# Performance work log

Measured on AMD Instinct MI355X. Metric: run time of the kernel, lower is better.

## Reference

```python
import jax, jax.numpy as jnp
import numpy as np

N_NODES = 50000
N_EDGES = 800000
IN_SIZE = 1024
EMB = 500


def setup_inputs() -> dict:
    key = jax.random.key(0)
    ks = jax.random.split(key, 9)
    x = jax.random.uniform(ks[0], (N_NODES, IN_SIZE), dtype=jnp.float32)
    edge_index = jax.random.randint(ks[1], (2, N_EDGES), 0, N_NODES, dtype=jnp.int32)
    edge_weight = jax.random.uniform(ks[2], (N_EDGES,), dtype=jnp.float32)
    s = 0.05
    wenc = jax.random.normal(ks[3], (EMB, IN_SIZE), dtype=jnp.float32) * s
    benc = jax.random.normal(ks[4], (EMB,), dtype=jnp.float32) * s
    wdec = jax.random.normal(ks[5], (IN_SIZE, EMB), dtype=jnp.float32) * s
    bdec = jax.random.normal(ks[6], (IN_SIZE,), dtype=jnp.float32) * s
    conv_weight = jax.random.normal(ks[7], (EMB, EMB), dtype=jnp.float32) * 0.1
    # lin.weight initialized N(0,0.1) + identity, per reset_parameters
    lin_weight = jax.random.normal(ks[8], (EMB, EMB), dtype=jnp.float32) * 0.1 + jnp.eye(EMB, dtype=jnp.float32)
    return {"x": x, "edge_index": edge_index, "edge_weight": edge_weight,
            "wenc": wenc, "benc": benc, "wdec": wdec, "bdec": bdec,
            "conv_weight": conv_weight, "lin_weight": lin_weight}


def reference(x, edge_index, edge_weight, wenc, benc, wdec, bdec, conv_weight, lin_weight):
    # encoder: h = sigmoid(x @ wenc^T + benc)          [N, EMB]
    h = jax.nn.sigmoid(x @ wenc.T + benc)
    # GraphConv (old PyG): neighbor transform then scatter-add to destinations
    h2 = h @ conv_weight                                # [N, EMB]
    src, dst = edge_index[0], edge_index[1]
    msgs = h2[src] * edge_weight[:, None]               # [E, EMB] gather + weight
    agg = jax.ops.segment_sum(msgs, dst, num_segments=x.shape[0])
    hout = agg + h @ lin_weight.T                       # root term via nn.Linear
    # decoder
    p = hout @ wdec.T + bdec                            # [N, IN_SIZE]
    return p
```

## Files before the change

kernel.cpp:

```cpp
#include <hip/hip_runtime.h>
#include <hip/hip_bf16.h>

typedef unsigned int u32;
typedef short bf16x8 __attribute__((ext_vector_type(8)));
typedef float floatx4 __attribute__((ext_vector_type(4)));

#define NNODES 50000
#define NEDGES 800000
#define INSZ   1024
#define EMB    500
#define EMBP   512

__device__ __forceinline__ short f2bf(float f) {
    u32 u = __builtin_bit_cast(u32, f);
    u32 r = u + 0x7FFFu + ((u >> 16) & 1u);
    return (short)(r >> 16);
}
__device__ __forceinline__ float bf2f(short h) {
    u32 u = ((u32)(unsigned short)h) << 16;
    return __builtin_bit_cast(float, u);
}

#define GLDS16(gp, lp) __builtin_amdgcn_global_load_lds( \
    (const __attribute__((address_space(1))) u32*)(gp),  \
    (__attribute__((address_space(3))) u32*)(lp), 16, 0, 0)

__device__ __forceinline__ u32 xcd_swz(u32 orig, u32 q, u32 r) {
    u32 xcd = orig & 7u, seq = orig >> 3;
    u32 base = (xcd < r) ? xcd * (q + 1u) : r * (q + 1u) + (xcd - r) * q;
    return base + seq;
}

__global__ void pack_all(const float* __restrict__ wenc, const float* __restrict__ conv,
                         const float* __restrict__ lin,  const float* __restrict__ wdec,
                         short* __restrict__ wencP, short* __restrict__ Wmid,
                         short* __restrict__ wdecP) {
    int tid = blockIdx.x * 256 + threadIdx.x;
    {
        int m = tid >> 10, k = tid & 1023;
        wencP[tid] = (m < EMB) ? f2bf(wenc[m * INSZ + k]) : (short)0;
    }
    {
        int m = tid >> 10, k = tid & 1023;
        short v = 0;
        if (m < EMB) {
            if (k < EMBP) { if (k < EMB) v = f2bf(conv[k * EMB + m]); }
            else          { int kk = k - EMBP; if (kk < EMB) v = f2bf(lin[m * EMB + kk]); }
        }
        Wmid[tid] = v;
    }
    {
        int m = tid >> 9, k = tid & 511;
        wdecP[tid] = (k < EMB) ? f2bf(wdec[m * EMB + k]) : (short)0;
    }
}

__global__ __launch_bounds__(256)
void conv_x(const float* __restrict__ X, short* __restrict__ Xb) {
    size_t base = ((size_t)blockIdx.x * 256 + threadIdx.x) * 8;
    floatx4 f0 = *(const floatx4*)(X + base);
    floatx4 f1 = *(const floatx4*)(X + base + 4);
    bf16x8 p;
#pragma unroll
    for (int j = 0; j < 4; ++j) { p[j] = f2bf(f0[j]); p[4 + j] = f2bf(f1[j]); }
    *(bf16x8*)(Xb + base) = p;
}


__global__ __launch_bounds__(256)
void gemm_enc(const short* __restrict__ Xb, const short* __restrict__ Wp,
              const float* __restrict__ benc, short* __restrict__ H) {
    __shared__ short As[2][128 * 32];
    __shared__ short Bs[2][128 * 32];
    const int tid  = threadIdx.x;
    const int lane = tid & 63;
    const int wave = tid >> 6;
    const int wr   = (wave >> 1) * 64;
    const int wc   = (wave & 1) * 64;
    const u32 swz  = xcd_swz(blockIdx.y * 4 + blockIdx.x, 195, 4);
    const int rowBase = (int)(swz >> 2) * 128;
    const int colBase = (int)(swz & 3) * 128;

    floatx4 acc[4][4] = {};

    const int r0 = tid >> 2;
    const int c0 = (tid & 3) * 8;
    int ar0 = rowBase + r0;       if (ar0 >= NNODES) ar0 = NNODES - 1;
    int ar1 = rowBase + r0 + 64;  if (ar1 >= NNODES) ar1 = NNODES - 1;
    const short* aP0 = Xb + (size_t)ar0 * INSZ + c0;
    const short* aP1 = Xb + (size_t)ar1 * INSZ + c0;
    const short* bP0 = Wp + (size_t)(colBase + r0) * INSZ + c0;
    const short* bP1 = Wp + (size_t)(colBase + r0 + 64) * INSZ + c0;

    const int q8  = (lane >> 4) * 8;
    const int m16 = lane & 15;

#define STAGE_E(buf, k0)                                   \
    GLDS16(aP0 + (k0), &As[buf][tid * 8]);                 \
    GLDS16(aP1 + (k0), &As[buf][2048 + tid * 8]);          \
    GLDS16(bP0 + (k0), &Bs[buf][tid * 8]);                 \
    GLDS16(bP1 + (k0), &Bs[buf][2048 + tid * 8]);

    STAGE_E(0, 0);
    __syncthreads();
    int cur = 0;
    for (int t = 0; t < 32; ++t) {
        if (t + 1 < 32) { STAGE_E(cur ^ 1, (t + 1) * 32); }
        bf16x8 af[4], bfr[4];
#pragma unroll
        for (int i = 0; i < 4; ++i) {
            af[i]  = *(const bf16x8*)&As[cur][(wr + i * 16 + m16) * 32 + q8];
            bfr[i] = *(const bf16x8*)&Bs[cur][(wc + i * 16 + m16) * 32 + q8];
        }
#pragma unroll
        for (int i = 0; i < 4; ++i)
#pragma unroll
            for (int j = 0; j < 4; ++j)
                acc[i][j] = __builtin_amdgcn_mfma_f32_16x16x32_bf16(af[i], bfr[j], acc[i][j], 0, 0, 0);
        __syncthreads();
        cur ^= 1;
    }
#undef STAGE_E

    const int rq = (lane >> 4) * 4;
#pragma unroll
    for (int i = 0; i < 4; ++i)
#pragma unroll
        for (int j = 0; j < 4; ++j)
#pragma unroll
            for (int reg = 0; reg < 4; ++reg) {
                int row = rowBase + wr + i * 16 + rq + reg;
                int col = colBase + wc + j * 16 + m16;
                if (row < NNODES) {
                    float b = (col < EMB) ? benc[col] : 0.f;
                    float v = 1.f / (1.f + __expf(-(acc[i][j][reg] + b)));
                    H[(size_t)row * EMBP + col] = f2bf(v);
                }
            }
}

__global__ __launch_bounds__(256)
void gemm_mid(const short* __restrict__ AggB, const short* __restrict__ H,
              const short* __restrict__ Wm, short* __restrict__ Hout) {
    __shared__ short As[2][128 * 32];
    __shared__ short Bs[2][128 * 32];
    const int tid  = threadIdx.x;
    const int lane = tid & 63;
    const int wave = tid >> 6;
    const int wr   = (wave >> 1) * 64;
    const int wc   = (wave & 1) * 64;
    const u32 swz  = xcd_swz(blockIdx.y * 4 + blockIdx.x, 195, 4);
    const int rowBase = (int)(swz >> 2) * 128;
    const int colBase = (int)(swz & 3) * 128;

    floatx4 acc[4][4] = {};

    const int r0 = tid >> 2;
    const int c0 = (tid & 3) * 8;
    int ar0 = rowBase + r0;       if (ar0 >= NNODES) ar0 = NNODES - 1;
    int ar1 = rowBase + r0 + 64;  if (ar1 >= NNODES) ar1 = NNODES - 1;
    const short* agP0 = AggB + (size_t)ar0 * EMBP + c0;
    const short* agP1 = AggB + (size_t)ar1 * EMBP + c0;
    const short* hP0  = H + (size_t)ar0 * EMBP + c0;
    const short* hP1  = H + (size_t)ar1 * EMBP + c0;
    const short* wP0  = Wm + (size_t)(colBase + r0) * 1024 + c0;
    const short* wP1  = Wm + (size_t)(colBase + r0 + 64) * 1024 + c0;

    const int q8  = (lane >> 4) * 8;
    const int m16 = lane & 15;

#define STAGE_M(buf, k0)                                              \
    if ((k0) < 512) {                                                 \
        GLDS16(agP0 + (k0), &As[buf][tid * 8]);                       \
        GLDS16(agP1 + (k0), &As[buf][2048 + tid * 8]);                \
    } else {                                                          \
        GLDS16(hP0 + ((k0) - 512), &As[buf][tid * 8]);                \
        GLDS16(hP1 + ((k0) - 512), &As[buf][2048 + tid * 8]);         \
    }                                                                 \
    GLDS16(wP0 + (k0), &Bs[buf][tid * 8]);                            \
    GLDS16(wP1 + (k0), &Bs[buf][2048 + tid * 8]);

    STAGE_M(0, 0);
    __syncthreads();
    int cur = 0;
    for (int t = 0; t < 32; ++t) {
        if (t + 1 < 32) { STAGE_M(cur ^ 1, (t + 1) * 32); }
        bf16x8 af[4], bfr[4];
#pragma unroll
        for (int i = 0; i < 4; ++i) {
            af[i]  = *(const bf16x8*)&As[cur][(wr + i * 16 + m16) * 32 + q8];
            bfr[i] = *(const bf16x8*)&Bs[cur][(wc + i * 16 + m16) * 32 + q8];
        }
#pragma unroll
        for (int i = 0; i < 4; ++i)
#pragma unroll
            for (int j = 0; j < 4; ++j)
                acc[i][j] = __builtin_amdgcn_mfma_f32_16x16x32_bf16(af[i], bfr[j], acc[i][j], 0, 0, 0);
        __syncthreads();
        cur ^= 1;
    }
#undef STAGE_M

    const int rq = (lane >> 4) * 4;
#pragma unroll
    for (int i = 0; i < 4; ++i)
#pragma unroll
        for (int j = 0; j < 4; ++j)
#pragma unroll
            for (int reg = 0; reg < 4; ++reg) {
                int row = rowBase + wr + i * 16 + rq + reg;
                int col = colBase + wc + j * 16 + m16;
                if (row < NNODES)
                    Hout[(size_t)row * EMBP + col] = f2bf(acc[i][j][reg]);
            }
}

__global__ __launch_bounds__(256)
void gemm_dec(const short* __restrict__ Hout, const short* __restrict__ Wd,
              const float* __restrict__ bdec, float* __restrict__ Out) {
    __shared__ short As[2][128 * 32];
    __shared__ short Bs[2][128 * 32];
    const int tid  = threadIdx.x;
    const int lane = tid & 63;
    const int wave = tid >> 6;
    const int wr   = (wave >> 1) * 64;
    const int wc   = (wave & 1) * 64;
    const u32 swz  = xcd_swz(blockIdx.y * 8 + blockIdx.x, 391, 0);
    const int rowBase = (int)(swz >> 3) * 128;
    const int colBase = (int)(swz & 7) * 128;

    floatx4 acc[4][4] = {};

    const int r0 = tid >> 2;
    const int c0 = (tid & 3) * 8;
    int ar0 = rowBase + r0;       if (ar0 >= NNODES) ar0 = NNODES - 1;
    int ar1 = rowBase + r0 + 64;  if (ar1 >= NNODES) ar1 = NNODES - 1;
    const short* aP0 = Hout + (size_t)ar0 * EMBP + c0;
    const short* aP1 = Hout + (size_t)ar1 * EMBP + c0;
    const short* bP0 = Wd + (size_t)(colBase + r0) * EMBP + c0;
    const short* bP1 = Wd + (size_t)(colBase + r0 + 64) * EMBP + c0;

    const int q8  = (lane >> 4) * 8;
    const int m16 = lane & 15;

#define STAGE_D(buf, k0)                                   \
    GLDS16(aP0 + (k0), &As[buf][tid * 8]);                 \
    GLDS16(aP1 + (k0), &As[buf][2048 + tid * 8]);          \
    GLDS16(bP0 + (k0), &Bs[buf][tid * 8]);                 \
    GLDS16(bP1 + (k0), &Bs[buf][2048 + tid * 8]);

    STAGE_D(0, 0);
    __syncthreads();
    int cur = 0;
    for (int t = 0; t < 16; ++t) {
        if (t + 1 < 16) { STAGE_D(cur ^ 1, (t + 1) * 32); }
        bf16x8 af[4], bfr[4];
#pragma unroll
        for (int i = 0; i < 4; ++i) {
            af[i]  = *(const bf16x8*)&As[cur][(wr + i * 16 + m16) * 32 + q8];
            bfr[i] = *(const bf16x8*)&Bs[cur][(wc + i * 16 + m16) * 32 + q8];
        }
#pragma unroll
        for (int i = 0; i < 4; ++i)
#pragma unroll
            for (int j = 0; j < 4; ++j)
                acc[i][j] = __builtin_amdgcn_mfma_f32_16x16x32_bf16(af[i], bfr[j], acc[i][j], 0, 0, 0);
        __syncthreads();
        cur ^= 1;
    }
#undef STAGE_D

    const int rq = (lane >> 4) * 4;
#pragma unroll
    for (int i = 0; i < 4; ++i)
#pragma unroll
        for (int j = 0; j < 4; ++j)
#pragma unroll
            for (int reg = 0; reg < 4; ++reg) {
                int row = rowBase + wr + i * 16 + rq + reg;
                int col = colBase + wc + j * 16 + m16;
                if (row < NNODES)
                    Out[(size_t)row * INSZ + col] = acc[i][j][reg] + bdec[col];
            }
}

__global__ __launch_bounds__(256)
void count_edges(const int* __restrict__ dst, int* __restrict__ counts) {
    int e = blockIdx.x * 256 + threadIdx.x;
    atomicAdd(&counts[dst[e]], 1);
}

__global__ __launch_bounds__(1024)
void scan_counts(const int* __restrict__ counts, int* __restrict__ rowPtr,
                 int* __restrict__ cursor) {
    __shared__ int wsum[16];
    __shared__ int sbase;
    const int t = threadIdx.x;
    const int lane = t & 63;
    const int wv = t >> 6;
    if (t == 0) sbase = 0;
    for (int chunk = 0; chunk < 50176; chunk += 1024) {
        int i = chunk + t;
        int c = (i < NNODES) ? counts[i] : 0;
        int v = c;
#pragma unroll
        for (int off = 1; off < 64; off <<= 1) {
            int u = __shfl_up(v, off, 64);
            if (lane >= off) v += u;
        }
        if (lane == 63) wsum[wv] = v;
        __syncthreads();
        int woff = 0, total = 0;
#pragma unroll
        for (int w = 0; w < 16; ++w) {
            int s = wsum[w];
            if (w < wv) woff += s;
            total += s;
        }
        int base = sbase;
        __syncthreads();
        if (i < NNODES) {
            int p = base + woff + v - c;
            rowPtr[i] = p;
            cursor[i] = p;
        }
        if (t == 0) sbase = base + total;
        __syncthreads();
    }
}

__global__ __launch_bounds__(256)
void fill_csr(const int* __restrict__ src, const int* __restrict__ dst,
              const float* __restrict__ ew, int* __restrict__ cursor,
              int* __restrict__ csrSrc, float* __restrict__ csrW) {
    int e = blockIdx.x * 256 + threadIdx.x;
    int d = dst[e];
    int p = atomicAdd(&cursor[d], 1);
    csrSrc[p] = src[e];
    csrW[p]   = ew[e];
}

__global__ __launch_bounds__(256)
void aggregate(const short* __restrict__ H, const int* __restrict__ rowPtr,
               const int* __restrict__ counts, const int* __restrict__ csrSrc,
               const float* __restrict__ csrW, short* __restrict__ aggB) {
    const int n    = blockIdx.x * 4 + (threadIdx.x >> 6);
    const int lane = threadIdx.x & 63;
    const int beg  = rowPtr[n];
    const int cnt  = counts[n];
    const short* hb = H + lane * 8;

    float acc[8] = {0.f, 0.f, 0.f, 0.f, 0.f, 0.f, 0.f, 0.f};
    int i = 0;
    for (; i + 4 <= cnt; i += 4) {
        int   s0 = csrSrc[beg + i],     s1 = csrSrc[beg + i + 1];
        int   s2 = csrSrc[beg + i + 2], s3 = csrSrc[beg + i + 3];
        float w0 = csrW[beg + i],       w1 = csrW[beg + i + 1];
        float w2 = csrW[beg + i + 2],   w3 = csrW[beg + i + 3];
        bf16x8 v0 = *(const bf16x8*)(hb + (size_t)s0 * EMBP);
        bf16x8 v1 = *(const bf16x8*)(hb + (size_t)s1 * EMBP);
        bf16x8 v2 = *(const bf16x8*)(hb + (size_t)s2 * EMBP);
        bf16x8 v3 = *(const bf16x8*)(hb + (size_t)s3 * EMBP);
#pragma unroll
        for (int j = 0; j < 8; ++j)
            acc[j] += w0 * bf2f(v0[j]) + w1 * bf2f(v1[j])
                    + w2 * bf2f(v2[j]) + w3 * bf2f(v3[j]);
    }
    for (; i < cnt; ++i) {
        int   s0 = csrSrc[beg + i];
        float w0 = csrW[beg + i];
        bf16x8 v0 = *(const bf16x8*)(hb + (size_t)s0 * EMBP);
#pragma unroll
        for (int j = 0; j < 8; ++j)
            acc[j] += w0 * bf2f(v0[j]);
    }

    bf16x8 o;
#pragma unroll
    for (int j = 0; j < 8; ++j) o[j] = f2bf(acc[j]);
    *(bf16x8*)(aggB + (size_t)n * EMBP + lane * 8) = o;
}

extern "C" void kernel_launch(void* const* d_in, const int* in_sizes, int n_in,
                              void* d_out, int out_size, void* d_ws, size_t ws_size,
                              hipStream_t stream) {
    const float* x    = (const float*)d_in[0];
    const int*   ei   = (const int*)d_in[1];
    const float* ew   = (const float*)d_in[2];
    const float* wenc = (const float*)d_in[3];
    const float* benc = (const float*)d_in[4];
    const float* wdec = (const float*)d_in[5];
    const float* bdec = (const float*)d_in[6];
    const float* conv = (const float*)d_in[7];
    const float* lin  = (const float*)d_in[8];
    float* out = (float*)d_out;

    char* ws = (char*)d_ws;
    short* wencP = (short*)(ws);
    short* Wmid  = (short*)(ws + 1048576);
    short* wdecP = (short*)(ws + 2097152);
    short* h     = (short*)(ws + 3145728);
    short* hout  = (short*)(ws + 3145728 + 51200000);

    short* aggB = (short*)d_out;
    short* Xbf  = (short*)((char*)d_out + 102400000);
    char*  scratch = (char*)d_out + 102400000;
    int*   counts = (int*)scratch;
    int*   rowPtr = counts + NNODES;
    int*   cursor = rowPtr + NNODES;
    int*   csrSrc = cursor + NNODES;
    float* csrW   = (float*)(csrSrc + NEDGES);

    dim3 blk(256);
    pack_all<<<2048, blk, 0, stream>>>(wenc, conv, lin, wdec, wencP, Wmid, wdecP);
    conv_x<<<25000, blk, 0, stream>>>(x, Xbf);

    int rowTiles = (NNODES + 127) / 128;

    gemm_enc<<<dim3(EMBP / 128, rowTiles), blk, 0, stream>>>(Xbf, wencP, benc, h);

    hipMemsetAsync(counts, 0, (size_t)NNODES * 4, stream);
    count_edges<<<NEDGES / 256, blk, 0, stream>>>(ei + NEDGES, counts);
    scan_counts<<<1, 1024, 0, stream>>>(counts, rowPtr, cursor);
    fill_csr<<<NEDGES / 256, blk, 0, stream>>>(ei, ei + NEDGES, ew, cursor, csrSrc, csrW);
    aggregate<<<NNODES / 4, blk, 0, stream>>>(h, rowPtr, counts, csrSrc, csrW, aggB);

    gemm_mid<<<dim3(EMBP / 128, rowTiles), blk, 0, stream>>>(aggB, h, Wmid, hout);

    gemm_dec<<<dim3(INSZ / 128, rowTiles), blk, 0, stream>>>(hout, wdecP, bdec, out);
}
```

Measured before the change: 930.1 us.

## Fold decoder weight into mid weights and fuse mid and decoder GEMMs

A small GEMM precomputes a combined 1024x1024 weight from the decoder weight and the stacked conv/lin weights. A single fused GEMM then multiplies [agg | h] (K=1024) straight into the output with the bias, replacing the separate mid and decoder GEMMs. This removes writing and re-reading the intermediate hout buffer and one launch, at the cost of a doubled K in the decoder-shaped GEMM and an extra bf16 rounding of the combined weight. The aggregation loop also gains an 8-wide unrolled gather to put more loads in flight.

```diff
diff --git a/kernel.cpp b/kernel.cpp
--- a/kernel.cpp
+++ b/kernel.cpp
@@ -33,25 +33,25 @@
 
 __global__ void pack_all(const float* __restrict__ wenc, const float* __restrict__ conv,
                          const float* __restrict__ lin,  const float* __restrict__ wdec,
-                         short* __restrict__ wencP, short* __restrict__ Wmid,
-                         short* __restrict__ wdecP) {
+                         short* __restrict__ wencP, short* __restrict__ wdecP,
+                         short* __restrict__ Bw) {
     int tid = blockIdx.x * 256 + threadIdx.x;
     {
         int m = tid >> 10, k = tid & 1023;
         wencP[tid] = (m < EMB) ? f2bf(wenc[m * INSZ + k]) : (short)0;
     }
     {
-        int m = tid >> 10, k = tid & 1023;
-        short v = 0;
-        if (m < EMB) {
-            if (k < EMBP) { if (k < EMB) v = f2bf(conv[k * EMB + m]); }
-            else          { int kk = k - EMBP; if (kk < EMB) v = f2bf(lin[m * EMB + kk]); }
-        }
-        Wmid[tid] = v;
-    }
-    {
         int m = tid >> 9, k = tid & 511;
         wdecP[tid] = (k < EMB) ? f2bf(wdec[m * EMB + k]) : (short)0;
+    }
+    {
+        int kk = tid >> 9, j = tid & 511;
+        short v = 0;
+        if (j < EMB) {
+            if (kk < EMB)                          v = f2bf(conv[kk * EMB + j]);
+            else if (kk >= 512 && kk - 512 < EMB)  v = f2bf(lin[j * EMB + (kk - 512)]);
+        }
+        Bw[tid] = v;
     }
 }
 
@@ -66,6 +66,71 @@
     *(bf16x8*)(Xb + base) = p;
 }
 
+
+__global__ __launch_bounds__(256)
+void gemm_wpre(const short* __restrict__ Ap, const short* __restrict__ Bp,
+               short* __restrict__ Wbig) {
+    __shared__ short As[2][128 * 32];
+    __shared__ short Bs[2][128 * 32];
+    const int tid  = threadIdx.x;
+    const int lane = tid & 63;
+    const int wave = tid >> 6;
+    const int wr   = (wave >> 1) * 64;
+    const int wc   = (wave & 1) * 64;
+    const int rowBase = blockIdx.y * 128;
+    const int colBase = blockIdx.x * 128;
+
+    floatx4 acc[4][4] = {};
+
+    const int r0 = tid >> 2;
+    const int c0 = (tid & 3) * 8;
+    const short* aP0 = Ap + (size_t)(rowBase + r0) * EMBP + c0;
+    const short* aP1 = Ap + (size_t)(rowBase + r0 + 64) * EMBP + c0;
+    const short* bP0 = Bp + (size_t)(colBase + r0) * EMBP + c0;
+    const short* bP1 = Bp + (size_t)(colBase + r0 + 64) * EMBP + c0;
+
+    const int q8  = (lane >> 4) * 8;
+    const int m16 = lane & 15;
+
+#define STAGE_W(buf, k0)                                   \
+    GLDS16(aP0 + (k0), &As[buf][tid * 8]);                 \
+    GLDS16(aP1 + (k0), &As[buf][2048 + tid * 8]);          \
+    GLDS16(bP0 + (k0), &Bs[buf][tid * 8]);                 \
+    GLDS16(bP1 + (k0), &Bs[buf][2048 + tid * 8]);
+
+    STAGE_W(0, 0);
+    __syncthreads();
+    int cur = 0;
+    for (int t = 0; t < 16; ++t) {
+        if (t + 1 < 16) { STAGE_W(cur ^ 1, (t + 1) * 32); }
+        bf16x8 af[4], bfr[4];
+#pragma unroll
+        for (int i = 0; i < 4; ++i) {
+            af[i]  = *(const bf16x8*)&As[cur][(wr + i * 16 + m16) * 32 + q8];
+            bfr[i] = *(const bf16x8*)&Bs[cur][(wc + i * 16 + m16) * 32 + q8];
+        }
+#pragma unroll
+        for (int i = 0; i < 4; ++i)
+#pragma unroll
+            for (int j = 0; j < 4; ++j)
+                acc[i][j] = __builtin_amdgcn_mfma_f32_16x16x32_bf16(af[i], bfr[j], acc[i][j], 0, 0, 0);
+        __syncthreads();
+        cur ^= 1;
+    }
+#undef STAGE_W
+
+    const int rq = (lane >> 4) * 4;
+#pragma unroll
+    for (int i = 0; i < 4; ++i)
+#pragma unroll
+        for (int j = 0; j < 4; ++j)
+#pragma unroll
+            for (int reg = 0; reg < 4; ++reg) {
+                int row = rowBase + wr + i * 16 + rq + reg;
+                int col = colBase + wc + j * 16 + m16;
+                Wbig[(size_t)row * 1024 + col] = f2bf(acc[i][j][reg]);
+            }
+}
 
 __global__ __launch_bounds__(256)
 void gemm_enc(const short* __restrict__ Xb, const short* __restrict__ Wp,
@@ -140,84 +205,9 @@
 }
 
 __global__ __launch_bounds__(256)
-void gemm_mid(const short* __restrict__ AggB, const short* __restrict__ H,
-              const short* __restrict__ Wm, short* __restrict__ Hout) {
-    __shared__ short As[2][128 * 32];
-    __shared__ short Bs[2][128 * 32];
-    const int tid  = threadIdx.x;
-    const int lane = tid & 63;
-    const int wave = tid >> 6;
-    const int wr   = (wave >> 1) * 64;
-    const int wc   = (wave & 1) * 64;
-    const u32 swz  = xcd_swz(blockIdx.y * 4 + blockIdx.x, 195, 4);
-    const int rowBase = (int)(swz >> 2) * 128;
-    const int colBase = (int)(swz & 3) * 128;
-
-    floatx4 acc[4][4] = {};
-
-    const int r0 = tid >> 2;
-    const int c0 = (tid & 3) * 8;
-    int ar0 = rowBase + r0;       if (ar0 >= NNODES) ar0 = NNODES - 1;
-    int ar1 = rowBase + r0 + 64;  if (ar1 >= NNODES) ar1 = NNODES - 1;
-    const short* agP0 = AggB + (size_t)ar0 * EMBP + c0;
-    const short* agP1 = AggB + (size_t)ar1 * EMBP + c0;
-    const short* hP0  = H + (size_t)ar0 * EMBP + c0;
-    const short* hP1  = H + (size_t)ar1 * EMBP + c0;
-    const short* wP0  = Wm + (size_t)(colBase + r0) * 1024 + c0;
-    const short* wP1  = Wm + (size_t)(colBase + r0 + 64) * 1024 + c0;
-
-    const int q8  = (lane >> 4) * 8;
-    const int m16 = lane & 15;
-
-#define STAGE_M(buf, k0)                                              \
-    if ((k0) < 512) {                                                 \
-        GLDS16(agP0 + (k0), &As[buf][tid * 8]);                       \
-        GLDS16(agP1 + (k0), &As[buf][2048 + tid * 8]);                \
-    } else {                                                          \
-        GLDS16(hP0 + ((k0) - 512), &As[buf][tid * 8]);                \
-        GLDS16(hP1 + ((k0) - 512), &As[buf][2048 + tid * 8]);         \
-    }                                                                 \
-    GLDS16(wP0 + (k0), &Bs[buf][tid * 8]);                            \
-    GLDS16(wP1 + (k0), &Bs[buf][2048 + tid * 8]);
-
-    STAGE_M(0, 0);
-    __syncthreads();
-    int cur = 0;
-    for (int t = 0; t < 32; ++t) {
-        if (t + 1 < 32) { STAGE_M(cur ^ 1, (t + 1) * 32); }
-        bf16x8 af[4], bfr[4];
-#pragma unroll
-        for (int i = 0; i < 4; ++i) {
-            af[i]  = *(const bf16x8*)&As[cur][(wr + i * 16 + m16) * 32 + q8];
-            bfr[i] = *(const bf16x8*)&Bs[cur][(wc + i * 16 + m16) * 32 + q8];
-        }
-#pragma unroll
-        for (int i = 0; i < 4; ++i)
-#pragma unroll
-            for (int j = 0; j < 4; ++j)
-                acc[i][j] = __builtin_amdgcn_mfma_f32_16x16x32_bf16(af[i], bfr[j], acc[i][j], 0, 0, 0);
-        __syncthreads();
-        cur ^= 1;
-    }
-#undef STAGE_M
-
-    const int rq = (lane >> 4) * 4;
-#pragma unroll
-    for (int i = 0; i < 4; ++i)
-#pragma unroll
-        for (int j = 0; j < 4; ++j)
-#pragma unroll
-            for (int reg = 0; reg < 4; ++reg) {
-                int row = rowBase + wr + i * 16 + rq + reg;
-                int col = colBase + wc + j * 16 + m16;
-                if (row < NNODES)
-                    Hout[(size_t)row * EMBP + col] = f2bf(acc[i][j][reg]);
-            }
-}
-
-__global__ __launch_bounds__(256)
-void gemm_dec(const short* __restrict__ Hout, const short* __restrict__ Wd,
-              const float* __restrict__ bdec, float* __restrict__ Out) {
+void gemm_fused(const short* __restrict__ AggB, const short* __restrict__ H,
+                const short* __restrict__ Wb, const float* __restrict__ bdec,
+                float* __restrict__ Out) {
     __shared__ short As[2][128 * 32];
     __shared__ short Bs[2][128 * 32];
     const int tid  = threadIdx.x;
@@ -235,25 +225,32 @@
     const int c0 = (tid & 3) * 8;
     int ar0 = rowBase + r0;       if (ar0 >= NNODES) ar0 = NNODES - 1;
     int ar1 = rowBase + r0 + 64;  if (ar1 >= NNODES) ar1 = NNODES - 1;
-    const short* aP0 = Hout + (size_t)ar0 * EMBP + c0;
-    const short* aP1 = Hout + (size_t)ar1 * EMBP + c0;
-    const short* bP0 = Wd + (size_t)(colBase + r0) * EMBP + c0;
-    const short* bP1 = Wd + (size_t)(colBase + r0 + 64) * EMBP + c0;
+    const short* agP0 = AggB + (size_t)ar0 * EMBP + c0;
+    const short* agP1 = AggB + (size_t)ar1 * EMBP + c0;
+    const short* hP0  = H + (size_t)ar0 * EMBP + c0;
+    const short* hP1  = H + (size_t)ar1 * EMBP + c0;
+    const short* wP0  = Wb + (size_t)(colBase + r0) * 1024 + c0;
+    const short* wP1  = Wb + (size_t)(colBase + r0 + 64) * 1024 + c0;
 
     const int q8  = (lane >> 4) * 8;
     const int m16 = lane & 15;
 
-#define STAGE_D(buf, k0)                                   \
-    GLDS16(aP0 + (k0), &As[buf][tid * 8]);                 \
-    GLDS16(aP1 + (k0), &As[buf][2048 + tid * 8]);          \
-    GLDS16(bP0 + (k0), &Bs[buf][tid * 8]);                 \
-    GLDS16(bP1 + (k0), &Bs[buf][2048 + tid * 8]);
-
-    STAGE_D(0, 0);
+#define STAGE_F(buf, k0)                                              \
+    if ((k0) < 512) {                                                 \
+        GLDS16(agP0 + (k0), &As[buf][tid * 8]);                       \
+        GLDS16(agP1 + (k0), &As[buf][2048 + tid * 8]);                \
+    } else {                                                          \
+        GLDS16(hP0 + ((k0) - 512), &As[buf][tid * 8]);                \
+        GLDS16(hP1 + ((k0) - 512), &As[buf][2048 + tid * 8]);         \
+    }                                                                 \
+    GLDS16(wP0 + (k0), &Bs[buf][tid * 8]);                            \
+    GLDS16(wP1 + (k0), &Bs[buf][2048 + tid * 8]);
+
+    STAGE_F(0, 0);
     __syncthreads();
     int cur = 0;
-    for (int t = 0; t < 16; ++t) {
-        if (t + 1 < 16) { STAGE_D(cur ^ 1, (t + 1) * 32); }
+    for (int t = 0; t < 32; ++t) {
+        if (t + 1 < 32) { STAGE_F(cur ^ 1, (t + 1) * 32); }
         bf16x8 af[4], bfr[4];
 #pragma unroll
         for (int i = 0; i < 4; ++i) {
@@ -268,7 +265,7 @@
         __syncthreads();
         cur ^= 1;
     }
-#undef STAGE_D
+#undef STAGE_F
 
     const int rq = (lane >> 4) * 4;
 #pragma unroll
@@ -352,19 +349,29 @@
 
     float acc[8] = {0.f, 0.f, 0.f, 0.f, 0.f, 0.f, 0.f, 0.f};
     int i = 0;
+    for (; i + 8 <= cnt; i += 8) {
+        int   s[8]; float w[8]; bf16x8 v[8];
+#pragma unroll
+        for (int u = 0; u < 8; ++u) { s[u] = csrSrc[beg + i + u]; w[u] = csrW[beg + i + u]; }
+#pragma unroll
+        for (int u = 0; u < 8; ++u) v[u] = *(const bf16x8*)(hb + (size_t)s[u] * EMBP);
+#pragma unroll
+        for (int u = 0; u < 8; ++u)
+#pragma unroll
+            for (int j = 0; j < 8; ++j)
+                acc[j] += w[u] * bf2f(v[u][j]);
+    }
     for (; i + 4 <= cnt; i += 4) {
-        int   s0 = csrSrc[beg + i],     s1 = csrSrc[beg + i + 1];
-        int   s2 = csrSrc[beg + i + 2], s3 = csrSrc[beg + i + 3];
-        float w0 = csrW[beg + i],       w1 = csrW[beg + i + 1];
-        float w2 = csrW[beg + i + 2],   w3 = csrW[beg + i + 3];
-        bf16x8 v0 = *(const bf16x8*)(hb + (size_t)s0 * EMBP);
-        bf16x8 v1 = *(const bf16x8*)(hb + (size_t)s1 * EMBP);
-        bf16x8 v2 = *(const bf16x8*)(hb + (size_t)s2 * EMBP);
-        bf16x8 v3 = *(const bf16x8*)(hb + (size_t)s3 * EMBP);
-#pragma unroll
-        for (int j = 0; j < 8; ++j)
-            acc[j] += w0 * bf2f(v0[j]) + w1 * bf2f(v1[j])
-                    + w2 * bf2f(v2[j]) + w3 * bf2f(v3[j]);
+        int   s[4]; float w[4]; bf16x8 v[4];
+#pragma unroll
+        for (int u = 0; u < 4; ++u) { s[u] = csrSrc[beg + i + u]; w[u] = csrW[beg + i + u]; }
+#pragma unroll
+        for (int u = 0; u < 4; ++u) v[u] = *(const bf16x8*)(hb + (size_t)s[u] * EMBP);
+#pragma unroll
+        for (int u = 0; u < 4; ++u)
+#pragma unroll
+            for (int j = 0; j < 8; ++j)
+                acc[j] += w[u] * bf2f(v[u][j]);
     }
     for (; i < cnt; ++i) {
         int   s0 = csrSrc[beg + i];
@@ -397,12 +404,12 @@
 
     char* ws = (char*)d_ws;
     short* wencP = (short*)(ws);
-    short* Wmid  = (short*)(ws + 1048576);
-    short* wdecP = (short*)(ws + 2097152);
-    short* h     = (short*)(ws + 3145728);
-    short* hout  = (short*)(ws + 3145728 + 51200000);
-
-    short* aggB = (short*)d_out;
+    short* wdecP = (short*)(ws + 1048576);
+    short* Bw    = (short*)(ws + 2097152);
+    short* Wbig  = (short*)(ws + 3145728);
+    short* h     = (short*)(ws + 5242880);
+    short* aggB  = (short*)(ws + 5242880 + 51200000);
+
     short* Xbf  = (short*)((char*)d_out + 102400000);
     char*  scratch = (char*)d_out + 102400000;
     int*   counts = (int*)scratch;
@@ -412,7 +419,10 @@
     float* csrW   = (float*)(csrSrc + NEDGES);
 
     dim3 blk(256);
-    pack_all<<<2048, blk, 0, stream>>>(wenc, conv, lin, wdec, wencP, Wmid, wdecP);
+    pack_all<<<2048, blk, 0, stream>>>(wenc, conv, lin, wdec, wencP, wdecP, Bw);
+
+    gemm_wpre<<<dim3(8, 8), blk, 0, stream>>>(wdecP, Bw, Wbig);
+
     conv_x<<<25000, blk, 0, stream>>>(x, Xbf);
 
     int rowTiles = (NNODES + 127) / 128;
@@ -425,7 +435,5 @@
     fill_csr<<<NEDGES / 256, blk, 0, stream>>>(ei, ei + NEDGES, ew, cursor, csrSrc, csrW);
     aggregate<<<NNODES / 4, blk, 0, stream>>>(h, rowPtr, counts, csrSrc, csrW, aggB);
 
-    gemm_mid<<<dim3(EMBP / 128, rowTiles), blk, 0, stream>>>(aggB, h, Wmid, hout);
-
-    gemm_dec<<<dim3(INSZ / 128, rowTiles), blk, 0, stream>>>(hout, wdecP, bdec, out);
-}
+    gemm_fused<<<dim3(INSZ / 128, rowTiles), blk, 0, stream>>>(aggB, h, Wbig, bdec, out);
+}
```

Result: no change. 917.5 us (-1.4%).
